# Optimization experiments

Measured on AMD Instinct MI355X. Metric: run time of the kernel, lower is better.

The kernel has to match this reference:

```python
import jax, jax.numpy as jnp
import numpy as np
import math

B, S, D, OUT, H = 512, 80, 768, 768, 12


def setup_inputs() -> dict:
    key = jax.random.key(0)
    ks = jax.random.split(key, 8)
    scale = 0.02
    hidden = jax.random.normal(ks[0], (B, S, D), dtype=jnp.float32)
    mask = jnp.ones((B, S), dtype=jnp.int32)
    Wq = jax.random.normal(ks[1], (D, D), dtype=jnp.float32) * scale
    bq = jax.random.normal(ks[2], (D,), dtype=jnp.float32) * scale
    Wk = jax.random.normal(ks[3], (D, D), dtype=jnp.float32) * scale
    bk = jax.random.normal(ks[4], (D,), dtype=jnp.float32) * scale
    Wv = jax.random.normal(ks[5], (D, OUT), dtype=jnp.float32) * scale
    bv = jax.random.normal(ks[6], (OUT,), dtype=jnp.float32) * scale
    return {"hidden": hidden, "mask": mask, "Wq": Wq, "bq": bq,
            "Wk": Wk, "bk": bk, "Wv": Wv, "bv": bv}


def _rope_tables(seq_len, head_dim, dtype):
    # RoE_QAndK(seq_len): standard RoPE, emb = cat([sin, cos], -1), chunked
    half = head_dim // 2
    inv_freq = 1.0 / (10000.0 ** (np.arange(0, half, dtype=np.float32) * 2.0 / head_dim))
    pos = np.arange(seq_len, dtype=np.float32)
    freqs = pos[:, None] * inv_freq[None, :]  # [S, half]
    return jnp.asarray(np.sin(freqs), dtype), jnp.asarray(np.cos(freqs), dtype)


def _rotate(x, sin, cos):
    # interleaved RoPE: even/odd channels
    x1, x2 = x[..., 0::2], x[..., 1::2]
    out = jnp.stack([x1 * cos - x2 * sin, x2 * cos + x1 * sin], axis=-1)
    return out.reshape(x.shape)


def reference(hidden, mask, Wq, bq, Wk, bk, Wv, bv):
    b, s, d = hidden.shape
    dh = Wq.shape[1] // H   # query/key head dim
    dv = Wv.shape[1] // H   # value head dim

    def split_heads(x, hd):
        return x.reshape(b, s, H, hd).transpose(0, 2, 1, 3)  # [b,h,s,hd]

    q = split_heads(hidden @ Wq + bq, dh)
    k = split_heads(hidden @ Wk + bk, dh)
    v = split_heads(hidden @ Wv + bv, dv)

    sin, cos = _rope_tables(s, dh, hidden.dtype)  # [s, dh//2]
    q = _rotate(q, sin, cos)
    k = _rotate(k, sin, cos)

    bias = (1.0 - mask.astype(hidden.dtype))[:, None, None, :] * -10000.0
    scores = jnp.einsum('bhqd,bhkd->bhqk', q, k) / math.sqrt(dh) + bias
    prob = jax.nn.softmax(scores, axis=-1)  # dropout is identity in eval
    ctx = jnp.einsum('bhqk,bhkd->bhqd', prob, v)
    return ctx.transpose(0, 2, 1, 3).reshape(b, s, H * dv)
```

## Files before the change

### kernel.cpp

```cpp
#include <hip/hip_runtime.h>
#include <hip/hip_bf16.h>
#include <stdint.h>

#define H_    12
#define B_    512
#define S_    80
#define D_    768
#define NQKV  2304
#define DH    64

typedef __bf16 bf16x8 __attribute__((ext_vector_type(8)));
typedef float  f32x4  __attribute__((ext_vector_type(4)));
typedef unsigned short u16;
typedef unsigned int   u32;

__device__ __forceinline__ u16 f2bf(float f) {
    u32 u = __builtin_bit_cast(u32, f);
    u32 r = u + 0x7FFFu + ((u >> 16) & 1u);
    return (u16)(r >> 16);
}
__device__ __forceinline__ float bf2f(u16 h) {
    u32 u = ((u32)h) << 16;
    return __builtin_bit_cast(float, u);
}

__device__ __forceinline__ void gload16(const void* g, void* l) {
    __builtin_amdgcn_global_load_lds((const __attribute__((address_space(1))) void*)g,
                                     (__attribute__((address_space(3))) void*)l, 16, 0, 0);
}

#define VMCNT(n) asm volatile("s_waitcnt vmcnt(" #n ")" ::: "memory")
#define BARRIER() do { asm volatile("" ::: "memory"); __builtin_amdgcn_s_barrier(); asm volatile("" ::: "memory"); } while (0)

#define TRB 432
#define CVB 1616

__global__ __launch_bounds__(256) void prep_fused(
    const float* __restrict__ X,
    const float* __restrict__ Wq, const float* __restrict__ bq,
    const float* __restrict__ Wk, const float* __restrict__ bk,
    const float* __restrict__ Wv, const float* __restrict__ bv,
    u16* __restrict__ Wt, float* __restrict__ biasf,
    float* __restrict__ ropeS, float* __restrict__ ropeC,
    u16* __restrict__ Xb)
{
    const int tid = threadIdx.x;
    if (blockIdx.x < TRB) {
        __shared__ u16 T[64][72];
        int t = blockIdx.x;
        int mat = t / 144;
        int rem = t - mat * 144;
        int kb = (rem / 12) * 64;
        int nb = (rem % 12) * 64;
        const float* W = (mat == 0) ? Wq : (mat == 1 ? Wk : Wv);
        int r  = tid >> 2;
        int q4 = tid & 3;
#pragma unroll
        for (int i = 0; i < 4; ++i) {
            float4 v = *reinterpret_cast<const float4*>(&W[(size_t)(kb + r) * D_ + nb + q4 * 16 + i * 4]);
            T[q4 * 16 + i * 4 + 0][r] = f2bf(v.x);
            T[q4 * 16 + i * 4 + 1][r] = f2bf(v.y);
            T[q4 * 16 + i * 4 + 2][r] = f2bf(v.z);
            T[q4 * 16 + i * 4 + 3][r] = f2bf(v.w);
        }
        __syncthreads();
        int n_local = tid >> 2;
        int kq = tid & 3;
        uint4 o0 = *reinterpret_cast<const uint4*>(&T[n_local][kq * 16]);
        uint4 o1 = *reinterpret_cast<const uint4*>(&T[n_local][kq * 16 + 8]);
        u16* dst = &Wt[(size_t)(mat * D_ + nb + n_local) * D_ + kb + kq * 16];
        *reinterpret_cast<uint4*>(dst) = o0;
        *reinterpret_cast<uint4*>(dst + 8) = o1;
    } else {
        int gidx = (blockIdx.x - TRB) * 256 + tid;
        const int gstride = CVB * 256;
        for (int i = gidx; i < NQKV; i += gstride) {
            const float* bsrc; int nn;
            if (i < D_)          { bsrc = bq; nn = i; }
            else if (i < 2 * D_) { bsrc = bk; nn = i - D_; }
            else                 { bsrc = bv; nn = i - 2 * D_; }
            biasf[i] = bsrc[nn];
        }
        for (int i = gidx; i < S_ * 32; i += gstride) {
            int pos = i >> 5, fi = i & 31;
            float invf = powf(10000.0f, -(float)fi / 32.0f);
            float fr = (float)pos * invf;
            ropeS[i] = sinf(fr);
            ropeC[i] = cosf(fr);
        }
        const int n4 = 40960 * D_ / 4;
        for (int i = gidx; i < n4; i += gstride) {
            float4 v = reinterpret_cast<const float4*>(X)[i];
            uint2 u;
            u.x = (u32)f2bf(v.x) | ((u32)f2bf(v.y) << 16);
            u.y = (u32)f2bf(v.z) | ((u32)f2bf(v.w) << 16);
            reinterpret_cast<uint2*>(Xb)[i] = u;
        }
    }
}

#define BK 64
#define NT 12
#define CLD 264

__global__ __launch_bounds__(512, 2) void qkv_gemm(
    const u16*   __restrict__ Xb,
    const u16*   __restrict__ Wt,
    const float* __restrict__ biasf,
    u16*         __restrict__ Y)
{
    __shared__ alignas(16) u16 smem[65536];

    const int orig = blockIdx.x;
    const int swz = (orig & 7) * 180 + (orig >> 3);
    const int m0 = (swz / 9) * 256;
    const int n0 = (swz % 9) * 256;

    const int tid = threadIdx.x;
    const int lane = tid & 63;
    const int w  = tid >> 6;
    const int wr = w >> 2;
    const int wc = w & 3;
    const int lr = lane & 15;
    const int lg = lane >> 4;

    const int srow = tid >> 3;
    const int scol = ((tid & 7) ^ (srow & 7)) << 3;

    f32x4 acc[8][4] = {};
    bf16x8 af[2][4], bf[2][4];

#define STAGE_A(p, h, q, kt) \
    gload16(&Xb[(size_t)(m0 + (h)*128 + (q)*64 + srow) * D_ + (kt)*BK + scol], \
            &smem[(p)*32768 + (h)*8192 + (q)*4096 + w*512])
#define STAGE_B(p, hb, jj, kt) \
    gload16(&Wt[(size_t)(n0 + (hb)*128 + (jj)*64 + srow) * D_ + (kt)*BK + scol], \
            &smem[(p)*32768 + 16384 + (hb)*8192 + (jj)*4096 + w*512])
#define LDA_F(p, rr, kk_) \
    (*reinterpret_cast<const bf16x8*>(&smem[(p)*32768 + wr*8192 + (rr)*64 + ((((kk_)*4 + lg) ^ ((rr) & 7)) << 3)]))
#define LDB_F(p, rb, kk_) \
    (*reinterpret_cast<const bf16x8*>(&smem[(p)*32768 + 16384 + (wc>>1)*8192 + (rb)*64 + ((((kk_)*4 + lg) ^ ((rb) & 7)) << 3)]))
#define STAGE_TILE(p, kt) do { \
    STAGE_A(p, 0, 0, kt); STAGE_A(p, 0, 1, kt); STAGE_A(p, 1, 0, kt); STAGE_A(p, 1, 1, kt); \
    STAGE_B(p, 0, 0, kt); STAGE_B(p, 0, 1, kt); STAGE_B(p, 1, 0, kt); STAGE_B(p, 1, 1, kt); } while (0)

    STAGE_TILE(0, 0);
    VMCNT(0);
    BARRIER();

#pragma unroll
    for (int u = 0; u < NT; ++u) {
        const int p = u & 1;
        if (u + 1 < NT) STAGE_TILE(p ^ 1, u + 1);

#pragma unroll
        for (int kk = 0; kk < 2; ++kk) {
#pragma unroll
            for (int ii = 0; ii < 4; ++ii) af[kk][ii] = LDA_F(p, ii * 16 + lr, kk);
#pragma unroll
            for (int jj = 0; jj < 2; ++jj) bf[kk][jj] = LDB_F(p, (wc & 1) * 64 + jj * 16 + lr, kk);
        }
#pragma unroll
        for (int kk = 0; kk < 2; ++kk)
#pragma unroll
            for (int ii = 0; ii < 4; ++ii)
#pragma unroll
                for (int jj = 0; jj < 2; ++jj)
                    acc[ii][jj] = __builtin_amdgcn_mfma_f32_16x16x32_bf16(af[kk][ii], bf[kk][jj], acc[ii][jj], 0, 0, 0);

#pragma unroll
        for (int kk = 0; kk < 2; ++kk)
#pragma unroll
            for (int jj = 2; jj < 4; ++jj) bf[kk][jj] = LDB_F(p, (wc & 1) * 64 + jj * 16 + lr, kk);
#pragma unroll
        for (int kk = 0; kk < 2; ++kk)
#pragma unroll
            for (int ii = 0; ii < 4; ++ii)
#pragma unroll
                for (int jj = 0; jj < 2; ++jj)
                    acc[ii][jj + 2] = __builtin_amdgcn_mfma_f32_16x16x32_bf16(af[kk][ii], bf[kk][jj + 2], acc[ii][jj + 2], 0, 0, 0);

#pragma unroll
        for (int kk = 0; kk < 2; ++kk)
#pragma unroll
            for (int ii = 0; ii < 4; ++ii) af[kk][ii] = LDA_F(p, 64 + ii * 16 + lr, kk);
#pragma unroll
        for (int kk = 0; kk < 2; ++kk)
#pragma unroll
            for (int ii = 0; ii < 4; ++ii)
#pragma unroll
                for (int jj = 0; jj < 2; ++jj)
                    acc[ii + 4][jj] = __builtin_amdgcn_mfma_f32_16x16x32_bf16(af[kk][ii], bf[kk][jj], acc[ii + 4][jj], 0, 0, 0);
#pragma unroll
        for (int kk = 0; kk < 2; ++kk)
#pragma unroll
            for (int ii = 0; ii < 4; ++ii)
#pragma unroll
                for (int jj = 0; jj < 2; ++jj)
                    acc[ii + 4][jj + 2] = __builtin_amdgcn_mfma_f32_16x16x32_bf16(af[kk][ii], bf[kk][jj + 2], acc[ii + 4][jj + 2], 0, 0, 0);

        VMCNT(0);
        BARRIER();
    }

    float bias_v[4];
#pragma unroll
    for (int j = 0; j < 4; ++j) bias_v[j] = biasf[n0 + wc * 64 + j * 16 + lr];

#pragma unroll
    for (int hh = 0; hh < 2; ++hh) {
        if (wr == hh) {
#pragma unroll
            for (int i = 0; i < 8; ++i)
#pragma unroll
                for (int j = 0; j < 4; ++j)
#pragma unroll
                    for (int r = 0; r < 4; ++r)
                        smem[(i * 16 + lg * 4 + r) * CLD + wc * 64 + j * 16 + lr] = f2bf(acc[i][j][r] + bias_v[j]);
        }
        __syncthreads();
#pragma unroll
        for (int pp = 0; pp < 8; ++pp) {
            int idx = pp * 512 + tid;
            int row = idx >> 5, ch = idx & 31;
            uint4 v = *reinterpret_cast<const uint4*>(&smem[row * CLD + ch * 8]);
            *reinterpret_cast<uint4*>(&Y[(size_t)(m0 + hh * 128 + row) * NQKV + n0 + ch * 8]) = v;
        }
        __syncthreads();
    }
#undef STAGE_A
#undef STAGE_B
#undef STAGE_TILE
#undef LDA_F
#undef LDB_F
}

#define LQ 72
#define LV 104

__device__ __forceinline__ u32 rope_rot(u32 u, float sn, float cs, float scale) {
    float x1 = bf2f((u16)(u & 0xffff)), x2 = bf2f((u16)(u >> 16));
    float o1 = (x1 * cs - x2 * sn) * scale;
    float o2 = (x2 * cs + x1 * sn) * scale;
    return (u32)f2bf(o1) | ((u32)f2bf(o2) << 16);
}

__global__ __launch_bounds__(320) void attn_kernel(
    const u16* __restrict__ Y,
    const int* __restrict__ mask,
    const float* __restrict__ ropeS,
    const float* __restrict__ ropeC,
    float* __restrict__ out)
{
    __shared__ alignas(16) u16 Qs[S_ * LQ];
    __shared__ alignas(16) u16 Ks[S_ * LQ];
    __shared__ alignas(16) u16 Vt[DH * LV];
    __shared__ alignas(16) u16 Ps[5 * 16 * LV];
    __shared__ float biasS[S_];

    const int h = blockIdx.x;
    const int b = blockIdx.y;
    const int tid = threadIdx.x;
    const size_t rowbase = (size_t)b * S_ * NQKV;

#pragma unroll
    for (int it = 0; it < 4; ++it) {
        int ch = it * 320 + tid;
        int q = ch >> 4;
        int sub = ch & 15;
        int isK = sub >> 3;
        int c0 = (sub & 7) * 8;
        uint4 v = *reinterpret_cast<const uint4*>(&Y[rowbase + (size_t)q * NQKV + isK * D_ + h * DH + c0]);
        float4 sn4 = *reinterpret_cast<const float4*>(&ropeS[q * 32 + c0 / 2]);
        float4 cs4 = *reinterpret_cast<const float4*>(&ropeC[q * 32 + c0 / 2]);
        float scale = isK ? 1.0f : 0.125f;
        uint4 o;
        o.x = rope_rot(v.x, sn4.x, cs4.x, scale);
        o.y = rope_rot(v.y, sn4.y, cs4.y, scale);
        o.z = rope_rot(v.z, sn4.z, cs4.z, scale);
        o.w = rope_rot(v.w, sn4.w, cs4.w, scale);
        u16* dst = isK ? Ks : Qs;
        *reinterpret_cast<uint4*>(&dst[q * LQ + c0]) = o;
    }
#pragma unroll
    for (int it = 0; it < 2; ++it) {
        int ch = it * 320 + tid;
        int s = ch >> 3, c0 = (ch & 7) * 8;
        uint4 v = *reinterpret_cast<const uint4*>(&Y[rowbase + (size_t)s * NQKV + 2 * D_ + h * DH + c0]);
        Vt[(c0 + 0) * LV + s] = (u16)(v.x & 0xffff);
        Vt[(c0 + 1) * LV + s] = (u16)(v.x >> 16);
        Vt[(c0 + 2) * LV + s] = (u16)(v.y & 0xffff);
        Vt[(c0 + 3) * LV + s] = (u16)(v.y >> 16);
        Vt[(c0 + 4) * LV + s] = (u16)(v.z & 0xffff);
        Vt[(c0 + 5) * LV + s] = (u16)(v.z >> 16);
        Vt[(c0 + 6) * LV + s] = (u16)(v.w & 0xffff);
        Vt[(c0 + 7) * LV + s] = (u16)(v.w >> 16);
    }
    for (int e = tid; e < DH * 16; e += 320) {
        int c = e >> 4, s = 80 + (e & 15);
        Vt[c * LV + s] = 0;
    }
    for (int e = tid; e < S_ * 16; e += 320) {
        int row = e >> 4, col = 80 + (e & 15);
        Ps[row * LV + col] = 0;
    }
    for (int e = tid; e < S_; e += 320)
        biasS[e] = (1.0f - (float)mask[b * S_ + e]) * -10000.0f;
    __syncthreads();

    const int wv = tid >> 6;
    const int lane = tid & 63;
    const int lr = lane & 15;
    const int lg = lane >> 4;

    f32x4 sc[5] = {};
    bf16x8 aq[2];
#pragma unroll
    for (int kk = 0; kk < 2; ++kk)
        aq[kk] = *reinterpret_cast<const bf16x8*>(&Qs[(wv * 16 + lr) * LQ + kk * 32 + lg * 8]);
#pragma unroll
    for (int t = 0; t < 5; ++t) {
#pragma unroll
        for (int kk = 0; kk < 2; ++kk) {
            bf16x8 bk8 = *reinterpret_cast<const bf16x8*>(&Ks[(t * 16 + lr) * LQ + kk * 32 + lg * 8]);
            sc[t] = __builtin_amdgcn_mfma_f32_16x16x32_bf16(aq[kk], bk8, sc[t], 0, 0, 0);
        }
    }
#pragma unroll
    for (int j = 0; j < 4; ++j) {
        float m = -1e30f;
#pragma unroll
        for (int t = 0; t < 5; ++t) { sc[t][j] += biasS[t * 16 + lr]; m = fmaxf(m, sc[t][j]); }
#pragma unroll
        for (int msk = 1; msk < 16; msk <<= 1) m = fmaxf(m, __shfl_xor(m, msk));
        float s = 0.f;
#pragma unroll
        for (int t = 0; t < 5; ++t) { float e = __expf(sc[t][j] - m); sc[t][j] = e; s += e; }
#pragma unroll
        for (int msk = 1; msk < 16; msk <<= 1) s += __shfl_xor(s, msk);
        float ri = 1.0f / s;
#pragma unroll
        for (int t = 0; t < 5; ++t) sc[t][j] *= ri;
    }
#pragma unroll
    for (int t = 0; t < 5; ++t)
#pragma unroll
        for (int j = 0; j < 4; ++j)
            Ps[(wv * 16 + lg * 4 + j) * LV + t * 16 + lr] = f2bf(sc[t][j]);
    __syncthreads();

    f32x4 co[4] = {};
#pragma unroll
    for (int kk = 0; kk < 3; ++kk) {
        bf16x8 ap = *reinterpret_cast<const bf16x8*>(&Ps[(wv * 16 + lr) * LV + kk * 32 + lg * 8]);
#pragma unroll
        for (int t = 0; t < 4; ++t) {
            bf16x8 bv8 = *reinterpret_cast<const bf16x8*>(&Vt[(t * 16 + lr) * LV + kk * 32 + lg * 8]);
            co[t] = __builtin_amdgcn_mfma_f32_16x16x32_bf16(ap, bv8, co[t], 0, 0, 0);
        }
    }
    const size_t obase = (size_t)(b * S_ + wv * 16 + lg * 4) * D_ + h * DH;
#pragma unroll
    for (int t = 0; t < 4; ++t)
#pragma unroll
        for (int j = 0; j < 4; ++j)
            out[obase + (size_t)j * D_ + t * 16 + lr] = co[t][j];
}

extern "C" void kernel_launch(void* const* d_in, const int* in_sizes, int n_in,
                              void* d_out, int out_size, void* d_ws, size_t ws_size,
                              hipStream_t stream) {
    const float* hidden = (const float*)d_in[0];
    const int*   mask   = (const int*)d_in[1];
    const float* Wq     = (const float*)d_in[2];
    const float* bq     = (const float*)d_in[3];
    const float* Wk     = (const float*)d_in[4];
    const float* bk     = (const float*)d_in[5];
    const float* Wv     = (const float*)d_in[6];
    const float* bv     = (const float*)d_in[7];
    float* out = (float*)d_out;

    char* ws = (char*)d_ws;
    u16*   Wt    = (u16*)(ws + 0);
    float* biasf = (float*)(ws + 3538944);
    float* ropeS = (float*)(ws + 3548160);
    float* ropeC = (float*)(ws + 3558400);
    u16*   Y     = (u16*)(ws + 4194304);

    u16* Xb = (u16*)d_out;

    prep_fused<<<dim3(TRB + CVB), dim3(256), 0, stream>>>(hidden, Wq, bq, Wk, bk, Wv, bv,
                                                          Wt, biasf, ropeS, ropeC, Xb);
    qkv_gemm<<<dim3(1440), dim3(512), 0, stream>>>(Xb, Wt, biasf, Y);
    attn_kernel<<<dim3(H_, B_), dim3(320), 0, stream>>>(Y, mask, ropeS, ropeC, out);
}
```

Before: 277.6 us.

## Restructure QKV GEMM main loop into barrier-phased ping-pong with setprio; stage attention output

The QKV projection GEMM main loop becomes a manually unrolled two-stage pipeline. Global-to-LDS loads for tile k+2 are issued in the middle of the MFMA groups, and fine-grained barriers, lgkmcnt waits and s_setprio wrap each MFMA group so waves interleave compute and memory. The attention kernel now stages its fp32 output tile in LDS, reusing the Q/K buffers, and writes it with 16-byte nontemporal stores instead of scattered scalar stores. The many extra barriers could add synchronisation overhead, and the schedule hard-codes the tile count.

```diff
diff --git a/kernel.cpp b/kernel.cpp
--- a/kernel.cpp
+++ b/kernel.cpp
@@ -30,6 +30,7 @@
 }
 
 #define VMCNT(n) asm volatile("s_waitcnt vmcnt(" #n ")" ::: "memory")
+#define LGKM0()  asm volatile("s_waitcnt lgkmcnt(0)" ::: "memory")
 #define BARRIER() do { asm volatile("" ::: "memory"); __builtin_amdgcn_s_barrier(); asm volatile("" ::: "memory"); } while (0)
 
 #define TRB 432
@@ -140,73 +141,98 @@
     (*reinterpret_cast<const bf16x8*>(&smem[(p)*32768 + wr*8192 + (rr)*64 + ((((kk_)*4 + lg) ^ ((rr) & 7)) << 3)]))
 #define LDB_F(p, rb, kk_) \
     (*reinterpret_cast<const bf16x8*>(&smem[(p)*32768 + 16384 + (wc>>1)*8192 + (rb)*64 + ((((kk_)*4 + lg) ^ ((rb) & 7)) << 3)]))
-#define STAGE_TILE(p, kt) do { \
-    STAGE_A(p, 0, 0, kt); STAGE_A(p, 0, 1, kt); STAGE_A(p, 1, 0, kt); STAGE_A(p, 1, 1, kt); \
-    STAGE_B(p, 0, 0, kt); STAGE_B(p, 0, 1, kt); STAGE_B(p, 1, 0, kt); STAGE_B(p, 1, 1, kt); } while (0)
-
-    STAGE_TILE(0, 0);
+
+#define READ_AQ0(p) { _Pragma("unroll") for (int kk = 0; kk < 2; ++kk) _Pragma("unroll") for (int ii = 0; ii < 4; ++ii) af[kk][ii] = LDA_F(p, ii * 16 + lr, kk); }
+#define READ_AQ1(p) { _Pragma("unroll") for (int kk = 0; kk < 2; ++kk) _Pragma("unroll") for (int ii = 0; ii < 4; ++ii) af[kk][ii] = LDA_F(p, 64 + ii * 16 + lr, kk); }
+#define READ_BJ01(p) { _Pragma("unroll") for (int kk = 0; kk < 2; ++kk) _Pragma("unroll") for (int jj = 0; jj < 2; ++jj) bf[kk][jj] = LDB_F(p, (wc & 1) * 64 + jj * 16 + lr, kk); }
+#define READ_BJ23(p) { _Pragma("unroll") for (int kk = 0; kk < 2; ++kk) _Pragma("unroll") for (int jj = 2; jj < 4; ++jj) bf[kk][jj] = LDB_F(p, (wc & 1) * 64 + jj * 16 + lr, kk); }
+#define MFMA_G(I0, J0) { __builtin_amdgcn_s_setprio(1); \
+    _Pragma("unroll") for (int kk = 0; kk < 2; ++kk) \
+    _Pragma("unroll") for (int ii = 0; ii < 4; ++ii) \
+    _Pragma("unroll") for (int jj = 0; jj < 2; ++jj) \
+        acc[(I0) + ii][(J0) + jj] = __builtin_amdgcn_mfma_f32_16x16x32_bf16(af[kk][ii], bf[kk][(J0) + jj], acc[(I0) + ii][(J0) + jj], 0, 0, 0); \
+    __builtin_amdgcn_s_setprio(0); }
+
+    STAGE_A(0, 0, 0, 0); STAGE_A(0, 0, 1, 0); STAGE_A(0, 1, 0, 0); STAGE_A(0, 1, 1, 0);
+    STAGE_B(0, 0, 0, 0); STAGE_B(0, 0, 1, 0); STAGE_B(0, 1, 0, 0); STAGE_B(0, 1, 1, 0);
+    STAGE_A(1, 0, 0, 1); STAGE_A(1, 0, 1, 1); STAGE_A(1, 1, 0, 1); STAGE_A(1, 1, 1, 1);
+    STAGE_B(1, 0, 0, 1); STAGE_B(1, 0, 1, 1); STAGE_B(1, 1, 0, 1); STAGE_B(1, 1, 1, 1);
+    VMCNT(8);
+    BARRIER();
+
+#pragma unroll
+    for (int u2 = 0; u2 < 5; ++u2) {
+        const int kt2 = 2 * u2 + 2, kt3 = 2 * u2 + 3;
+        READ_AQ0(0); READ_BJ01(0);
+        BARRIER(); LGKM0();
+        MFMA_G(0, 0);
+        BARRIER();
+        READ_BJ23(0);
+        BARRIER(); LGKM0();
+        MFMA_G(0, 2);
+        BARRIER();
+        READ_AQ1(0);
+        BARRIER(); LGKM0();
+        MFMA_G(4, 0);
+        BARRIER();
+        STAGE_A(0, 0, 0, kt2); STAGE_A(0, 0, 1, kt2); STAGE_A(0, 1, 0, kt2); STAGE_A(0, 1, 1, kt2);
+        VMCNT(4);
+        BARRIER();
+        MFMA_G(4, 2);
+        BARRIER();
+        READ_AQ0(1); READ_BJ01(1);
+        STAGE_B(0, 0, 0, kt2); STAGE_B(0, 0, 1, kt2); STAGE_B(0, 1, 0, kt2); STAGE_B(0, 1, 1, kt2);
+        BARRIER(); LGKM0();
+        MFMA_G(0, 0);
+        BARRIER();
+        READ_BJ23(1);
+        BARRIER(); LGKM0();
+        MFMA_G(0, 2);
+        BARRIER();
+        READ_AQ1(1);
+        BARRIER(); LGKM0();
+        MFMA_G(4, 0);
+        BARRIER();
+        STAGE_A(1, 0, 0, kt3); STAGE_A(1, 0, 1, kt3); STAGE_A(1, 1, 0, kt3); STAGE_A(1, 1, 1, kt3);
+        STAGE_B(1, 0, 0, kt3); STAGE_B(1, 0, 1, kt3); STAGE_B(1, 1, 0, kt3); STAGE_B(1, 1, 1, kt3);
+        VMCNT(8);
+        BARRIER();
+        MFMA_G(4, 2);
+        BARRIER();
+    }
+
+    READ_AQ0(0); READ_BJ01(0);
+    BARRIER(); LGKM0();
+    MFMA_G(0, 0);
+    BARRIER();
+    READ_BJ23(0);
+    BARRIER(); LGKM0();
+    MFMA_G(0, 2);
+    BARRIER();
+    READ_AQ1(0);
+    BARRIER(); LGKM0();
+    MFMA_G(4, 0);
+    BARRIER();
     VMCNT(0);
     BARRIER();
-
-#pragma unroll
-    for (int u = 0; u < NT; ++u) {
-        const int p = u & 1;
-        if (u + 1 < NT) STAGE_TILE(p ^ 1, u + 1);
-
-#pragma unroll
-        for (int kk = 0; kk < 2; ++kk) {
-#pragma unroll
-            for (int ii = 0; ii < 4; ++ii) af[kk][ii] = LDA_F(p, ii * 16 + lr, kk);
-#pragma unroll
-            for (int jj = 0; jj < 2; ++jj) bf[kk][jj] = LDB_F(p, (wc & 1) * 64 + jj * 16 + lr, kk);
-        }
-#pragma unroll
-        for (int kk = 0; kk < 2; ++kk)
-#pragma unroll
-            for (int ii = 0; ii < 4; ++ii)
-#pragma unroll
-                for (int jj = 0; jj < 2; ++jj)
-                    acc[ii][jj] = __builtin_amdgcn_mfma_f32_16x16x32_bf16(af[kk][ii], bf[kk][jj], acc[ii][jj], 0, 0, 0);
-
-#pragma unroll
-        for (int kk = 0; kk < 2; ++kk)
-#pragma unroll
-            for (int jj = 2; jj < 4; ++jj) bf[kk][jj] = LDB_F(p, (wc & 1) * 64 + jj * 16 + lr, kk);
-#pragma unroll
-        for (int kk = 0; kk < 2; ++kk)
-#pragma unroll
-            for (int ii = 0; ii < 4; ++ii)
-#pragma unroll
-                for (int jj = 0; jj < 2; ++jj)
-                    acc[ii][jj + 2] = __builtin_amdgcn_mfma_f32_16x16x32_bf16(af[kk][ii], bf[kk][jj + 2], acc[ii][jj + 2], 0, 0, 0);
-
-#pragma unroll
-        for (int kk = 0; kk < 2; ++kk)
-#pragma unroll
-            for (int ii = 0; ii < 4; ++ii) af[kk][ii] = LDA_F(p, 64 + ii * 16 + lr, kk);
-#pragma unroll
-        for (int kk = 0; kk < 2; ++kk)
-#pragma unroll
-            for (int ii = 0; ii < 4; ++ii)
-#pragma unroll
-                for (int jj = 0; jj < 2; ++jj)
-                    acc[ii + 4][jj] = __builtin_amdgcn_mfma_f32_16x16x32_bf16(af[kk][ii], bf[kk][jj], acc[ii + 4][jj], 0, 0, 0);
-#pragma unroll
-        for (int kk = 0; kk < 2; ++kk)
-#pragma unroll
-            for (int ii = 0; ii < 4; ++ii)
-#pragma unroll
-                for (int jj = 0; jj < 2; ++jj)
-                    acc[ii + 4][jj + 2] = __builtin_amdgcn_mfma_f32_16x16x32_bf16(af[kk][ii], bf[kk][jj + 2], acc[ii + 4][jj + 2], 0, 0, 0);
-
-        VMCNT(0);
-        BARRIER();
-    }
+    MFMA_G(4, 2);
+    BARRIER();
+    READ_AQ0(1); READ_BJ01(1);
+    LGKM0();
+    MFMA_G(0, 0);
+    READ_BJ23(1);
+    LGKM0();
+    MFMA_G(0, 2);
+    READ_AQ1(1);
+    LGKM0();
+    MFMA_G(4, 0);
+    MFMA_G(4, 2);
 
     float bias_v[4];
 #pragma unroll
     for (int j = 0; j < 4; ++j) bias_v[j] = biasf[n0 + wc * 64 + j * 16 + lr];
 
+    __syncthreads();
 #pragma unroll
     for (int hh = 0; hh < 2; ++hh) {
         if (wr == hh) {
@@ -230,13 +256,18 @@
     }
 #undef STAGE_A
 #undef STAGE_B
-#undef STAGE_TILE
 #undef LDA_F
 #undef LDB_F
+#undef READ_AQ0
+#undef READ_AQ1
+#undef READ_BJ01
+#undef READ_BJ23
+#undef MFMA_G
 }
 
 #define LQ 72
 #define LV 104
+#define LO 68
 
 __device__ __forceinline__ u32 rope_rot(u32 u, float sn, float cs, float scale) {
     float x1 = bf2f((u16)(u & 0xffff)), x2 = bf2f((u16)(u >> 16));
@@ -252,11 +283,13 @@
     const float* __restrict__ ropeC,
     float* __restrict__ out)
 {
-    __shared__ alignas(16) u16 Qs[S_ * LQ];
-    __shared__ alignas(16) u16 Ks[S_ * LQ];
+    __shared__ alignas(16) u16 pool[2 * S_ * LQ];
     __shared__ alignas(16) u16 Vt[DH * LV];
     __shared__ alignas(16) u16 Ps[5 * 16 * LV];
     __shared__ float biasS[S_];
+    u16* Qs = pool;
+    u16* Ks = pool + S_ * LQ;
+    float* Os = reinterpret_cast<float*>(pool);
 
     const int h = blockIdx.x;
     const int b = blockIdx.y;
@@ -359,12 +392,19 @@
             co[t] = __builtin_amdgcn_mfma_f32_16x16x32_bf16(ap, bv8, co[t], 0, 0, 0);
         }
     }
-    const size_t obase = (size_t)(b * S_ + wv * 16 + lg * 4) * D_ + h * DH;
 #pragma unroll
     for (int t = 0; t < 4; ++t)
 #pragma unroll
         for (int j = 0; j < 4; ++j)
-            out[obase + (size_t)j * D_ + t * 16 + lr] = co[t][j];
+            Os[(wv * 16 + lg * 4 + j) * LO + t * 16 + lr] = co[t][j];
+    __syncthreads();
+#pragma unroll
+    for (int it = 0; it < 4; ++it) {
+        int idx = it * 320 + tid;
+        int row = idx >> 4, c4 = (idx & 15) * 4;
+        f32x4 v = *reinterpret_cast<const f32x4*>(&Os[row * LO + c4]);
+        __builtin_nontemporal_store(v, reinterpret_cast<f32x4*>(&out[(size_t)(b * S_ + row) * D_ + h * DH + c4]));
+    }
 }
 
 extern "C" void kernel_launch(void* const* d_in, const int* in_sizes, int n_in,
```

New measurement: 286.7 us. 3.3% more time.
